# Kernel tuning notes

Hardware: AMD Instinct MI355X
Metric: run time of the kernel (lower is better)

## Reference

```python
import jax, jax.numpy as jnp
import numpy as np

B, S, F = 1024, 1000, 63   # batch, seq_len, raw features
H = 512                    # hidden_size
OUT = 2                    # output_size (num_weights_mode=0, GRID_DATA=False)
TRUNC = 100                # truncation_len


def _linear_init(k, fan_in, fan_out):
    bound = 1.0 / np.sqrt(fan_in)
    kw, kb = jax.random.split(k)
    W = jax.random.uniform(kw, (fan_in, fan_out), jnp.float32, -bound, bound)
    b = jax.random.uniform(kb, (fan_out,), jnp.float32, -bound, bound)
    return W, b


def setup_inputs() -> dict:
    key = jax.random.key(0)
    ks = jax.random.split(key, 5)
    x = jax.random.normal(ks[0], (B, S, F), jnp.float32)
    W = jax.random.normal(ks[1], (B, 1, OUT), jnp.float32)
    in_dim = OUT + F - 1  # 64: concat(W_state, x[:, t, 1:])
    W1, b1 = _linear_init(ks[2], in_dim, H)
    W2, b2 = _linear_init(ks[3], H, H)
    W3, b3 = _linear_init(ks[4], H, OUT)
    scaling_factor = jnp.full((OUT,), 0.001, jnp.float32)
    return dict(x=x, W=W, scaling_factor=scaling_factor,
                W1=W1, b1=b1, W2=W2, b2=b2, W3=W3, b3=b3)


def reference(x, W, scaling_factor, W1, b1, W2, b2, W3, b3):
    Bx, Sx, Fx = x.shape
    nchunks = Sx // TRUNC
    # (nchunks, TRUNC, B, F) for chunked scan (matches truncated-BPTT chunking)
    xs = x.transpose(1, 0, 2).reshape(nchunks, TRUNC, Bx, Fx)
    W0 = W[:, 0, :]  # (B, OUT)

    def mlp(z):
        h = jax.nn.relu(z @ W1 + b1)
        h = jax.nn.relu(h @ W2 + b2)
        return h @ W3 + b3

    def step(Wc, xt):
        z = jnp.concatenate([Wc, xt[:, 1:]], axis=-1)  # (B, OUT+F-1)
        dW = scaling_factor * mlp(z)                   # (B, OUT)
        Wn = Wc + dW
        return Wn, (Wn, dW)

    def chunk(Wc, xch):
        Wn, ys = jax.lax.scan(step, Wc, xch)
        # W.detach() at chunk boundary (no-op for forward values)
        return jax.lax.stop_gradient(Wn), ys

    _, (Ws, dWs) = jax.lax.scan(chunk, W0, xs)
    outputs = Ws.reshape(Sx, Bx, OUT).transpose(1, 0, 2)  # (B, S, OUT)
    # num_weights_mode == 0 readout
    weighted_sum = outputs[:, :, 0] * x[:, :, 0] + outputs[:, :, -1]
    sigmoid_output = jax.nn.sigmoid(weighted_sum)[..., None]  # (B, S, 1)
    dW_last = dWs[-1, -1]  # (B, OUT), last timestep's dW
    return sigmoid_output, dW_last, outputs
```

## Files before the change

### kernel.cpp

```cpp
#include <hip/hip_runtime.h>
#include <hip/hip_bf16.h>

#define B_ 1024
#define S_ 1000
#define F_ 63
#define H_ 512
#define OUT_ 2
#define M_ 16
#define NBLK (B_ / M_)
#define THREADS 512
#define NWAVE 8

typedef __attribute__((ext_vector_type(8))) __bf16 bf16x8;
typedef __attribute__((ext_vector_type(4))) float f32x4;
static_assert(sizeof(bf16x8) == 16, "bf16x8 must be 16B");

__device__ __forceinline__ unsigned short f2bf(float f) {
  union { float f; unsigned u; } v; v.f = f;
  unsigned r = v.u + 0x7FFF + ((v.u >> 16) & 1);
  return (unsigned short)(r >> 16);
}
__device__ __forceinline__ unsigned packbf(float a, float b) {
  return (unsigned)f2bf(a) | ((unsigned)f2bf(b) << 16);
}

__global__ void k_prep_w2(const float* __restrict__ W2, unsigned short* __restrict__ W2t) {
  __shared__ float tile[64][65];
  int bx = blockIdx.x & 7, by = blockIdx.x >> 3;
  int r0 = by * 64, c0 = bx * 64;
  for (int rep = 0; rep < 16; rep++) {
    int idx = rep * 256 + threadIdx.x;
    int i = idx >> 6, j = idx & 63;
    tile[i][j] = W2[(r0 + i) * 512 + (c0 + j)];
  }
  __syncthreads();
  for (int rep = 0; rep < 16; rep++) {
    int idx = rep * 256 + threadIdx.x;
    int i = idx >> 6, j = idx & 63;
    W2t[(c0 + i) * 512 + (r0 + j)] = f2bf(tile[j][i]);
  }
}

__global__ __launch_bounds__(THREADS)
void k_scan(const float* __restrict__ x, const float* __restrict__ W0in,
            const float* __restrict__ sf, const float* __restrict__ W1,
            const float* __restrict__ b1, const unsigned short* __restrict__ W2t,
            const float* __restrict__ b2, const float* __restrict__ W3,
            const float* __restrict__ b3, float* __restrict__ out)
{
  __shared__ __attribute__((aligned(16))) unsigned short w1t[512 * 64];
  __shared__ __attribute__((aligned(16))) unsigned short zA[2][16 * 64];
  __shared__ __attribute__((aligned(16))) unsigned short h1A[16 * 512];
  __shared__ __attribute__((aligned(16))) float b1s[512];
  __shared__ __attribute__((aligned(16))) float b2s[512];
  __shared__ float2 w3s[512];
  __shared__ float2 dwred[NWAVE][16];
  __shared__ float2 wst[16];
  __shared__ float x0s[2][16];
  __shared__ float cons[4];

  const int tid  = threadIdx.x;
  const int wid  = tid >> 6;
  const int lane = tid & 63;
  const int lr   = lane & 15;
  const int g    = lane >> 4;
  const int b0   = blockIdx.x * M_;

  {
    int n = tid;
    for (int k = 0; k < 64; k += 2) {
      float a = W1[k * 512 + n];
      float c = W1[(k + 1) * 512 + n];
      int off = n * 128 + (((k ^ ((n & 7) << 3))) << 1);
      *(unsigned*)((char*)w1t + off) = packbf(a, c);
    }
    b1s[tid] = b1[tid];
    b2s[tid] = b2[tid];
    w3s[tid] = make_float2(W3[tid * 2], W3[tid * 2 + 1]);
  }
  if (tid < 16) {
    float w0v = W0in[(b0 + tid) * 2], w1v = W0in[(b0 + tid) * 2 + 1];
    wst[tid] = make_float2(w0v, w1v);
    int off = tid * 128 + ((tid & 7) << 4);
    *(unsigned*)((char*)zA + off) = packbf(w0v, w1v);
  }
  {
    int r = tid >> 5, l32 = tid & 31;
    long xb = (long)(b0 + r) * (S_ * F_);
    if (l32 < 31) {
      float a = x[xb + 1 + 2 * l32];
      float c = x[xb + 2 + 2 * l32];
      int k = 2 + 2 * l32;
      int off = r * 128 + ((k ^ ((r & 7) << 3)) << 1);
      *(unsigned*)((char*)zA + off) = packbf(a, c);
    } else {
      x0s[0][r] = x[xb];
    }
  }
  if (tid < 4) cons[tid] = (tid < 2) ? b3[tid] : sf[tid - 2];
  __syncthreads();

  float* out_sig = out;
  float* out_dwl = out + (long)B_ * S_;
  float* out_ws  = out + (long)B_ * S_ + B_ * OUT_;

  for (int t = 0; t < S_; t++) {
    const int cur = t & 1, nxt = cur ^ 1;

    const int r5 = tid >> 5, l32 = tid & 31;
    float pf0 = 0.f, pf1 = 0.f, px0 = 0.f;
    if (t + 1 < S_) {
      long xb = (long)(b0 + r5) * (S_ * F_) + (long)(t + 1) * F_;
      if (l32 < 31) { pf0 = x[xb + 1 + 2 * l32]; pf1 = x[xb + 2 + 2 * l32]; }
      else          { px0 = x[xb]; }
    }

    const char* zb = (const char*)zA + cur * 2048;
    bf16x8 bz0, bz1;
    {
      int o0 = lr * 128 + (((g * 8)      ^ ((lr & 7) << 3)) << 1);
      int o1 = lr * 128 + (((32 + g * 8) ^ ((lr & 7) << 3)) << 1);
      bz0 = __builtin_bit_cast(bf16x8, *(const int4*)(zb + o0));
      bz1 = __builtin_bit_cast(bf16x8, *(const int4*)(zb + o1));
    }
#pragma unroll
    for (int mt = 0; mt < 4; mt++) {
      int n1b = wid * 64 + mt * 16;
      int n1  = n1b + lr;
      int oa0 = n1 * 128 + (((g * 8)      ^ ((n1 & 7) << 3)) << 1);
      int oa1 = n1 * 128 + (((32 + g * 8) ^ ((n1 & 7) << 3)) << 1);
      bf16x8 a0 = __builtin_bit_cast(bf16x8, *(const int4*)((const char*)w1t + oa0));
      bf16x8 a1 = __builtin_bit_cast(bf16x8, *(const int4*)((const char*)w1t + oa1));
      f32x4 acc = {0.f, 0.f, 0.f, 0.f};
      acc = __builtin_amdgcn_mfma_f32_16x16x32_bf16(a0, bz0, acc, 0, 0, 0);
      acc = __builtin_amdgcn_mfma_f32_16x16x32_bf16(a1, bz1, acc, 0, 0, 0);
      int nr = n1b + g * 4;
      float4 bb = *(const float4*)&b1s[nr];
      float h0 = fmaxf(acc[0] + bb.x, 0.f);
      float h1v = fmaxf(acc[1] + bb.y, 0.f);
      float h2v = fmaxf(acc[2] + bb.z, 0.f);
      float h3 = fmaxf(acc[3] + bb.w, 0.f);
      unsigned lo = packbf(h0, h1v), hi = packbf(h2v, h3);
      int ow = lr * 1024 + ((nr ^ ((lr & 7) << 3)) << 1);
      *(unsigned long long*)((char*)h1A + ow) =
          (unsigned long long)lo | ((unsigned long long)hi << 32);
    }
    __syncthreads();

    bf16x8 bh[16];
#pragma unroll
    for (int kt = 0; kt < 16; kt++) {
      int n = kt * 32 + g * 8;
      int o = lr * 1024 + ((n ^ ((lr & 7) << 3)) << 1);
      bh[kt] = __builtin_bit_cast(bf16x8, *(const int4*)((const char*)h1A + o));
    }
    float dw0 = 0.f, dw1 = 0.f;
#pragma unroll
    for (int mt = 0; mt < 4; mt++) {
      int n2b = wid * 64 + mt * 16;
      int n2  = n2b + lr;
      const char* wrow = (const char*)W2t + ((long)n2 * 512 + g * 8) * 2;
      f32x4 acc = {0.f, 0.f, 0.f, 0.f};
#pragma unroll
      for (int kt = 0; kt < 16; kt++) {
        bf16x8 a = __builtin_bit_cast(bf16x8, *(const int4*)(wrow + kt * 64));
        acc = __builtin_amdgcn_mfma_f32_16x16x32_bf16(a, bh[kt], acc, 0, 0, 0);
      }
      int nr = n2b + g * 4;
      float4 bb = *(const float4*)&b2s[nr];
      float bba[4] = {bb.x, bb.y, bb.z, bb.w};
#pragma unroll
      for (int i = 0; i < 4; i++) {
        float h = fmaxf(acc[i] + bba[i], 0.f);
        float2 w3v = w3s[nr + i];
        dw0 += h * w3v.x;
        dw1 += h * w3v.y;
      }
    }
    dw0 += __shfl_xor(dw0, 16); dw1 += __shfl_xor(dw1, 16);
    dw0 += __shfl_xor(dw0, 32); dw1 += __shfl_xor(dw1, 32);
    if (lane < 16) dwred[wid][lane] = make_float2(dw0, dw1);
    __syncthreads();

    if (wid == 0 && lane < 16) {
      int r = lane;
      float s0 = 0.f, s1 = 0.f;
#pragma unroll
      for (int w = 0; w < NWAVE; w++) { float2 p = dwred[w][r]; s0 += p.x; s1 += p.y; }
      float d0 = (s0 + cons[0]) * cons[2];
      float d1 = (s1 + cons[1]) * cons[3];
      float2 wc = wst[r];
      float w0n = wc.x + d0, w1n = wc.y + d1;
      wst[r] = make_float2(w0n, w1n);
      long oi = (long)(b0 + r) * S_ + t;
      out_ws[oi * 2]     = w0n;
      out_ws[oi * 2 + 1] = w1n;
      float zv = w0n * x0s[cur][r] + w1n;
      out_sig[oi] = 1.f / (1.f + expf(-zv));
      if (t == S_ - 1) { out_dwl[(b0 + r) * 2] = d0; out_dwl[(b0 + r) * 2 + 1] = d1; }
      if (t + 1 < S_) {
        int off = nxt * 2048 + r * 128 + ((r & 7) << 4);
        *(unsigned*)((char*)zA + off) = packbf(w0n, w1n);
      }
    }
    if (t + 1 < S_) {
      char* znb = (char*)zA + nxt * 2048;
      if (l32 < 31) {
        int k = 2 + 2 * l32;
        int off = r5 * 128 + ((k ^ ((r5 & 7) << 3)) << 1);
        *(unsigned*)(znb + off) = packbf(pf0, pf1);
      } else {
        x0s[nxt][r5] = px0;
      }
    }
    __syncthreads();
  }
}

extern "C" void kernel_launch(void* const* d_in, const int* in_sizes, int n_in,
                              void* d_out, int out_size, void* d_ws, size_t ws_size,
                              hipStream_t stream) {
  const float* x  = (const float*)d_in[0];
  const float* W0 = (const float*)d_in[1];
  const float* sf = (const float*)d_in[2];
  const float* W1 = (const float*)d_in[3];
  const float* b1 = (const float*)d_in[4];
  const float* W2 = (const float*)d_in[5];
  const float* b2 = (const float*)d_in[6];
  const float* W3 = (const float*)d_in[7];
  const float* b3 = (const float*)d_in[8];
  unsigned short* W2t = (unsigned short*)d_ws;
  float* out = (float*)d_out;

  k_prep_w2<<<dim3(64), dim3(256), 0, stream>>>(W2, W2t);
  k_scan<<<dim3(NBLK), dim3(THREADS), 0, stream>>>(x, W0, sf, W1, b1, W2t, b2, W3, b3, out);
}
```

Baseline: 6.887 ms.

## Keep W1 and part of W2 in registers and LDS, stream the rest

New measurement: 8.686 ms. 26.1% more time.

```diff
diff --git a/kernel.cpp b/kernel.cpp
--- a/kernel.cpp
+++ b/kernel.cpp
@@ -23,6 +23,9 @@
 __device__ __forceinline__ unsigned packbf(float a, float b) {
   return (unsigned)f2bf(a) | ((unsigned)f2bf(b) << 16);
 }
+__device__ __forceinline__ bf16x8 ld16(const void* p) {
+  return __builtin_bit_cast(bf16x8, *(const int4*)p);
+}
 
 __global__ void k_prep_w2(const float* __restrict__ W2, unsigned short* __restrict__ W2t) {
   __shared__ float tile[64][65];
@@ -48,12 +51,12 @@
             const float* __restrict__ b2, const float* __restrict__ W3,
             const float* __restrict__ b3, float* __restrict__ out)
 {
-  __shared__ __attribute__((aligned(16))) unsigned short w1t[512 * 64];
+  __shared__ __attribute__((aligned(16))) unsigned short w2l[128 * 512];
+  __shared__ __attribute__((aligned(16))) unsigned short h1A[16 * 512];
   __shared__ __attribute__((aligned(16))) unsigned short zA[2][16 * 64];
-  __shared__ __attribute__((aligned(16))) unsigned short h1A[16 * 512];
   __shared__ __attribute__((aligned(16))) float b1s[512];
   __shared__ __attribute__((aligned(16))) float b2s[512];
-  __shared__ float2 w3s[512];
+  __shared__ unsigned w3p[512];
   __shared__ float2 dwred[NWAVE][16];
   __shared__ float2 wst[16];
   __shared__ float x0s[2][16];
@@ -66,18 +69,43 @@
   const int g    = lane >> 4;
   const int b0   = blockIdx.x * M_;
 
+  bf16x8 w1f[4][2];
+#pragma unroll
+  for (int mt = 0; mt < 4; mt++) {
+    int n1 = wid * 64 + mt * 16 + lr;
+#pragma unroll
+    for (int ks = 0; ks < 2; ks++) {
+      union { bf16x8 v; unsigned short s[8]; } tmp;
+#pragma unroll
+      for (int j = 0; j < 8; j++)
+        tmp.s[j] = f2bf(W1[(ks * 32 + g * 8 + j) * 512 + n1]);
+      w1f[mt][ks] = tmp.v;
+    }
+  }
+  bf16x8 w2f0[16];
   {
-    int n = tid;
-    for (int k = 0; k < 64; k += 2) {
-      float a = W1[k * 512 + n];
-      float c = W1[(k + 1) * 512 + n];
-      int off = n * 128 + (((k ^ ((n & 7) << 3))) << 1);
-      *(unsigned*)((char*)w1t + off) = packbf(a, c);
-    }
-    b1s[tid] = b1[tid];
-    b2s[tid] = b2[tid];
-    w3s[tid] = make_float2(W3[tid * 2], W3[tid * 2 + 1]);
-  }
+    const char* r0p = (const char*)W2t + ((long)(wid * 64 + lr) * 512 + g * 8) * 2;
+#pragma unroll
+    for (int kt = 0; kt < 16; kt++) w2f0[kt] = ld16(r0p + kt * 64);
+  }
+  const char* p2 = (const char*)W2t + ((long)(wid * 64 + 32 + lr) * 512 + g * 8) * 2;
+  const char* p3 = (const char*)W2t + ((long)(wid * 64 + 48 + lr) * 512 + g * 8) * 2;
+  int4 A2a[8], A3a[8];
+#pragma unroll
+  for (int j = 0; j < 8; j++) { A2a[j] = *(const int4*)(p2 + j * 64); A3a[j] = *(const int4*)(p3 + j * 64); }
+  {
+    int R = tid >> 2, q = tid & 3;
+    int w = R >> 4, r16 = R & 15;
+    const char* src = (const char*)W2t + ((long)(w * 64 + 16 + r16) * 512) * 2 + q * 256;
+#pragma unroll
+    for (int c = 0; c < 16; c++) {
+      int kb = q * 256 + c * 16;
+      *(int4*)((char*)w2l + R * 1024 + (kb ^ ((R & 7) << 4))) = *(const int4*)(src + c * 16);
+    }
+  }
+  b1s[tid] = b1[tid];
+  b2s[tid] = b2[tid];
+  w3p[tid] = packbf(W3[tid * 2], W3[tid * 2 + 1]);
   if (tid < 16) {
     float w0v = W0in[(b0 + tid) * 2], w1v = W0in[(b0 + tid) * 2 + 1];
     wst[tid] = make_float2(w0v, w1v);
@@ -104,6 +132,9 @@
   float* out_dwl = out + (long)B_ * S_;
   float* out_ws  = out + (long)B_ * S_ + B_ * OUT_;
 
+  const int R   = wid * 16 + lr;
+  const int swR = (R & 7) << 4;
+
   for (int t = 0; t < S_; t++) {
     const int cur = t & 1, nxt = cur ^ 1;
 
@@ -120,20 +151,15 @@
     {
       int o0 = lr * 128 + (((g * 8)      ^ ((lr & 7) << 3)) << 1);
       int o1 = lr * 128 + (((32 + g * 8) ^ ((lr & 7) << 3)) << 1);
-      bz0 = __builtin_bit_cast(bf16x8, *(const int4*)(zb + o0));
-      bz1 = __builtin_bit_cast(bf16x8, *(const int4*)(zb + o1));
+      bz0 = ld16(zb + o0);
+      bz1 = ld16(zb + o1);
     }
 #pragma unroll
     for (int mt = 0; mt < 4; mt++) {
       int n1b = wid * 64 + mt * 16;
-      int n1  = n1b + lr;
-      int oa0 = n1 * 128 + (((g * 8)      ^ ((n1 & 7) << 3)) << 1);
-      int oa1 = n1 * 128 + (((32 + g * 8) ^ ((n1 & 7) << 3)) << 1);
-      bf16x8 a0 = __builtin_bit_cast(bf16x8, *(const int4*)((const char*)w1t + oa0));
-      bf16x8 a1 = __builtin_bit_cast(bf16x8, *(const int4*)((const char*)w1t + oa1));
       f32x4 acc = {0.f, 0.f, 0.f, 0.f};
-      acc = __builtin_amdgcn_mfma_f32_16x16x32_bf16(a0, bz0, acc, 0, 0, 0);
-      acc = __builtin_amdgcn_mfma_f32_16x16x32_bf16(a1, bz1, acc, 0, 0, 0);
+      acc = __builtin_amdgcn_mfma_f32_16x16x32_bf16(w1f[mt][0], bz0, acc, 0, 0, 0);
+      acc = __builtin_amdgcn_mfma_f32_16x16x32_bf16(w1f[mt][1], bz1, acc, 0, 0, 0);
       int nr = n1b + g * 4;
       float4 bb = *(const float4*)&b1s[nr];
       float h0 = fmaxf(acc[0] + bb.x, 0.f);
@@ -147,34 +173,55 @@
     }
     __syncthreads();
 
-    bf16x8 bh[16];
-#pragma unroll
-    for (int kt = 0; kt < 16; kt++) {
+    f32x4 acc0 = {0.f,0.f,0.f,0.f}, acc1 = acc0, acc2 = acc0, acc3 = acc0;
+#pragma unroll
+    for (int kt = 0; kt < 8; kt++) {
       int n = kt * 32 + g * 8;
-      int o = lr * 1024 + ((n ^ ((lr & 7) << 3)) << 1);
-      bh[kt] = __builtin_bit_cast(bf16x8, *(const int4*)((const char*)h1A + o));
-    }
+      bf16x8 bh = ld16((const char*)h1A + lr * 1024 + ((n ^ ((lr & 7) << 3)) << 1));
+      int kb = kt * 64 + g * 16;
+      bf16x8 a1 = ld16((const char*)w2l + R * 1024 + (kb ^ swR));
+      bf16x8 a2 = __builtin_bit_cast(bf16x8, A2a[kt]);
+      bf16x8 a3 = __builtin_bit_cast(bf16x8, A3a[kt]);
+      acc0 = __builtin_amdgcn_mfma_f32_16x16x32_bf16(w2f0[kt], bh, acc0, 0, 0, 0);
+      acc1 = __builtin_amdgcn_mfma_f32_16x16x32_bf16(a1, bh, acc1, 0, 0, 0);
+      acc2 = __builtin_amdgcn_mfma_f32_16x16x32_bf16(a2, bh, acc2, 0, 0, 0);
+      acc3 = __builtin_amdgcn_mfma_f32_16x16x32_bf16(a3, bh, acc3, 0, 0, 0);
+      A2a[kt] = *(const int4*)(p2 + (kt + 8) * 64);
+      A3a[kt] = *(const int4*)(p3 + (kt + 8) * 64);
+    }
+#pragma unroll
+    for (int kt = 8; kt < 16; kt++) {
+      int n = kt * 32 + g * 8;
+      bf16x8 bh = ld16((const char*)h1A + lr * 1024 + ((n ^ ((lr & 7) << 3)) << 1));
+      int kb = kt * 64 + g * 16;
+      bf16x8 a1 = ld16((const char*)w2l + R * 1024 + (kb ^ swR));
+      bf16x8 a2 = __builtin_bit_cast(bf16x8, A2a[kt - 8]);
+      bf16x8 a3 = __builtin_bit_cast(bf16x8, A3a[kt - 8]);
+      acc0 = __builtin_amdgcn_mfma_f32_16x16x32_bf16(w2f0[kt], bh, acc0, 0, 0, 0);
+      acc1 = __builtin_amdgcn_mfma_f32_16x16x32_bf16(a1, bh, acc1, 0, 0, 0);
+      acc2 = __builtin_amdgcn_mfma_f32_16x16x32_bf16(a2, bh, acc2, 0, 0, 0);
+      acc3 = __builtin_amdgcn_mfma_f32_16x16x32_bf16(a3, bh, acc3, 0, 0, 0);
+      A2a[kt - 8] = *(const int4*)(p2 + (kt - 8) * 64);
+      A3a[kt - 8] = *(const int4*)(p3 + (kt - 8) * 64);
+    }
+
     float dw0 = 0.f, dw1 = 0.f;
-#pragma unroll
-    for (int mt = 0; mt < 4; mt++) {
-      int n2b = wid * 64 + mt * 16;
-      int n2  = n2b + lr;
-      const char* wrow = (const char*)W2t + ((long)n2 * 512 + g * 8) * 2;
-      f32x4 acc = {0.f, 0.f, 0.f, 0.f};
-#pragma unroll
-      for (int kt = 0; kt < 16; kt++) {
-        bf16x8 a = __builtin_bit_cast(bf16x8, *(const int4*)(wrow + kt * 64));
-        acc = __builtin_amdgcn_mfma_f32_16x16x32_bf16(a, bh[kt], acc, 0, 0, 0);
-      }
-      int nr = n2b + g * 4;
-      float4 bb = *(const float4*)&b2s[nr];
-      float bba[4] = {bb.x, bb.y, bb.z, bb.w};
-#pragma unroll
-      for (int i = 0; i < 4; i++) {
-        float h = fmaxf(acc[i] + bba[i], 0.f);
-        float2 w3v = w3s[nr + i];
-        dw0 += h * w3v.x;
-        dw1 += h * w3v.y;
+    {
+      const f32x4 accs[4] = {acc0, acc1, acc2, acc3};
+#pragma unroll
+      for (int mt = 0; mt < 4; mt++) {
+        int nr = wid * 64 + mt * 16 + g * 4;
+        float4 bb = *(const float4*)&b2s[nr];
+        float bba[4] = {bb.x, bb.y, bb.z, bb.w};
+#pragma unroll
+        for (int i = 0; i < 4; i++) {
+          float h = fmaxf(accs[mt][i] + bba[i], 0.f);
+          unsigned u = w3p[nr + i];
+          float w3x = __uint_as_float((u & 0xFFFFu) << 16);
+          float w3y = __uint_as_float(u & 0xFFFF0000u);
+          dw0 += h * w3x;
+          dw1 += h * w3y;
+        }
       }
     }
     dw0 += __shfl_xor(dw0, 16); dw1 += __shfl_xor(dw1, 16);
@@ -196,7 +243,7 @@
       out_ws[oi * 2]     = w0n;
       out_ws[oi * 2 + 1] = w1n;
       float zv = w0n * x0s[cur][r] + w1n;
-      out_sig[oi] = 1.f / (1.f + expf(-zv));
+      out_sig[oi] = 1.f / (1.f + __expf(-zv));
       if (t == S_ - 1) { out_dwl[(b0 + r) * 2] = d0; out_dwl[(b0 + r) * 2 + 1] = d1; }
       if (t + 1 < S_) {
         int off = nxt * 2048 + r * 128 + ((r & 7) << 4);
```
